# Optimization experiments

Measured on AMD Instinct MI355X. Metric: run time of the kernel, lower is better.

## Reference

```python
import jax, jax.numpy as jnp
import numpy as np

BS, SEQ, D, HEADS = 4, 512, 512, 8

def setup_inputs() -> dict:
    key = jax.random.key(0)
    ks = jax.random.split(key, 11)
    s = 0.02
    return {
        "q": jax.random.normal(ks[0], (BS, SEQ, D), jnp.float32),
        "k": jax.random.normal(ks[1], (BS, SEQ, D), jnp.float32),
        "v": jax.random.normal(ks[2], (BS, SEQ, D), jnp.float32),
        "wq_w": jax.random.normal(ks[3], (D * HEADS, D), jnp.float32) * s,
        "wq_b": jax.random.normal(ks[4], (D * HEADS,), jnp.float32) * s,
        "wk_w": jax.random.normal(ks[5], (D * HEADS, D), jnp.float32) * s,
        "wk_b": jax.random.normal(ks[6], (D * HEADS,), jnp.float32) * s,
        "wv_w": jax.random.normal(ks[7], (D * HEADS, D), jnp.float32) * s,
        "wv_b": jax.random.normal(ks[8], (D * HEADS,), jnp.float32) * s,
        "out_w": jax.random.normal(ks[9], (D, D * HEADS), jnp.float32) * s,
        "out_b": jax.random.normal(ks[10], (D,), jnp.float32) * s,
    }

def reference(q, k, v, wq_w, wq_b, wk_w, wk_b, wv_w, wv_b, out_w, out_b):
    bs, _, d = q.shape
    heads = wq_w.shape[0] // d
    # NOTE: original code applies self.wk to q and self.wq to k (swapped) -- kept faithful.
    # Projections map (bs, seq, d) -> (bs, seq*heads, d): heads folded into sequence axis.
    qp = (q @ wk_w.T + wk_b).reshape(bs, -1, d)  # (bs, L, d), L = seq*heads
    kp = (k @ wq_w.T + wq_b).reshape(bs, -1, d)
    vp = (v @ wv_w.T + wv_b).reshape(bs, -1, d)
    scale = jnp.float32(np.sqrt(d))
    scores = jnp.einsum('bld,bmd->blm', qp, kp) / scale  # (bs, L, L)
    attn = jax.nn.softmax(scores, axis=-1)
    o = jnp.einsum('blm,bmd->bld', attn, vp)             # (bs, L, d)
    o = o.reshape(bs, -1, d * heads)                      # (bs, seq, d*heads)
    return o @ out_w.T + out_b                            # (bs, seq, d)
```

## Files before the change

kernel.cpp:

```cpp
#include <hip/hip_runtime.h>
#include <cstddef>

typedef unsigned short u16;
typedef unsigned char u8;
typedef unsigned u32;
typedef float f32x4 __attribute__((ext_vector_type(4)));
typedef u16 u16x4 __attribute__((ext_vector_type(4)));
typedef u16 u16x8 __attribute__((ext_vector_type(8)));
typedef u8 u8x8 __attribute__((ext_vector_type(8)));
typedef __bf16 bf16x8 __attribute__((ext_vector_type(8)));
typedef int i32x4 __attribute__((ext_vector_type(4)));
typedef int i32x8 __attribute__((ext_vector_type(8)));
typedef long lx2 __attribute__((ext_vector_type(2)));

__device__ __forceinline__ u16 f2bf(float f) {
  u32 u = __builtin_bit_cast(u32, f);
  u += 0x7fffu + ((u >> 16) & 1u);
  return (u16)(u >> 16);
}
__device__ __forceinline__ float bf2f(u16 h) {
  return __builtin_bit_cast(float, ((u32)h) << 16);
}
__device__ __forceinline__ u8 f2fp8(float v) {
  int t = __builtin_amdgcn_cvt_pk_fp8_f32(v, v, 0, false);
  return (u8)(t & 0xff);
}
__device__ __forceinline__ void gld_lds16(const void* g, void* l) {
  __builtin_amdgcn_global_load_lds((const __attribute__((address_space(1))) void*)g,
                                   (__attribute__((address_space(3))) void*)l, 16, 0, 0);
}

__global__ __launch_bounds__(256) void cvt_all(
    const float* __restrict__ q, const float* __restrict__ k, const float* __restrict__ v,
    const float* __restrict__ w5, const float* __restrict__ w3,
    const float* __restrict__ w7, const float* __restrict__ w9,
    u16* __restrict__ o_q, u16* __restrict__ o_k, u16* __restrict__ o_v,
    u16* __restrict__ o_wq, u16* __restrict__ o_wk, u16* __restrict__ o_wv,
    u16* __restrict__ o_ow)
{
  int b = blockIdx.x;
  const float* in; u16* out; int base; bool perm = false;
  if      (b < 512)  { in = q;  out = o_q;  base = b; }
  else if (b < 1024) { in = k;  out = o_k;  base = b - 512; }
  else if (b < 1536) { in = v;  out = o_v;  base = b - 1024; }
  else if (b < 2560) { in = w5; out = o_wq; base = b - 1536; }
  else if (b < 3584) { in = w3; out = o_wk; base = b - 2560; }
  else if (b < 4608) { in = w7; out = o_wv; base = b - 3584; }
  else               { in = w9; out = o_ow; base = b - 4608; perm = true; }
  int i = (base * 256 + threadIdx.x) * 8;
  u16x8 o;
  if (!perm) {
    f32x4 a = *(const f32x4*)(in + i);
    f32x4 c = *(const f32x4*)(in + i + 4);
    o[0] = f2bf(a[0]); o[1] = f2bf(a[1]); o[2] = f2bf(a[2]); o[3] = f2bf(a[3]);
    o[4] = f2bf(c[0]); o[5] = f2bf(c[1]); o[6] = f2bf(c[2]); o[7] = f2bf(c[3]);
  } else {
    int row = i >> 12, col0 = i & 4095;
    int group = col0 & ~63, t0 = col0 & 63;
    const float* rp = in + ((size_t)row << 12) + group;
#pragma unroll
    for (int j = 0; j < 8; ++j) {
      int t = t0 + j;
      o[j] = f2bf(rp[((t & 3) << 4) + (t >> 2)]);
    }
  }
  *(u16x8*)(out + i) = o;
}

__global__ __launch_bounds__(256, 2) void gemm_proj(
    const u16* __restrict__ Aq, const u16* __restrict__ Ak, const u16* __restrict__ Av,
    const u16* __restrict__ Bq, const u16* __restrict__ Bk, const u16* __restrict__ Bv,
    u8* __restrict__ Cq, u8* __restrict__ Ck, u8* __restrict__ Cvv,
    const float* __restrict__ bq, const float* __restrict__ bk, const float* __restrict__ bv,
    int N, int K)
{
  __shared__ alignas(16) char smem[33024];

  const int tid = threadIdx.x, lid = tid & 63, wid = tid >> 6;
  const int wm = wid >> 1, wn = wid & 1;
  const int g = lid >> 4, r16 = lid & 15;
  const int which = blockIdx.z;

  const u16* A = (which == 0) ? Aq : (which == 1) ? Ak : Av;
  const u16* B = (which == 0) ? Bq : (which == 1) ? Bk : Bv;
  u8* C = (which == 0) ? Cq : (which == 1) ? Ck : Cvv;
  const float* bias = (which == 0) ? bq : (which == 1) ? bk : bv;

  const int nx = gridDim.x, ny = gridDim.y;
  const int lin = blockIdx.x + nx * blockIdx.y;
  const int xcd = lin & 7, slot = lin >> 3;
  const int wx = slot % nx;
  const int c_ = xcd + (slot / nx) * 8;
  const int m0 = (c_ % ny) * 128, n0 = wx * 128;

  const int NT = K >> 5;

  int offA[4], offB[4];
#pragma unroll
  for (int f = 0; f < 4; ++f) {
    int ra = wm * 64 + f * 16 + r16;
    offA[f] = ra * 64 + ((g ^ ((ra >> 1) & 3)) << 4);
    int rb = wn * 64 + f * 16 + r16;
    offB[f] = rb * 64 + ((g ^ ((rb >> 1) & 3)) << 4);
  }

  auto stage_tile = [&](int ts) {
    char* base = smem + (ts & 1) * 16384;
    const u16* At = A + (size_t)ts * 32;
    const u16* Bt = B + (size_t)ts * 32;
#pragma unroll
    for (int l = 0; l < 2; ++l) {
      int i = l * 256 + tid;
      int row = i >> 2, x = i & 3;
      int c = x ^ ((row >> 1) & 3);
      gld_lds16(At + (size_t)(m0 + row) * K + c * 8, base + i * 16);
    }
#pragma unroll
    for (int l = 0; l < 2; ++l) {
      int i = l * 256 + tid;
      int row = i >> 2, x = i & 3;
      int c = x ^ ((row >> 1) & 3);
      gld_lds16(Bt + (size_t)(n0 + row) * K + c * 8, base + 8192 + i * 16);
    }
  };

  f32x4 acc[4][4];
#pragma unroll
  for (int i = 0; i < 4; ++i)
#pragma unroll
    for (int j = 0; j < 4; ++j) acc[i][j] = 0.0f;

  stage_tile(0);
  stage_tile(1);
  asm volatile("s_waitcnt vmcnt(4)" ::: "memory");
  __builtin_amdgcn_s_barrier();

  for (int t = 0; t < NT; ++t) {
    const char* Ab = smem + (t & 1) * 16384;
    const char* Bb = Ab + 8192;
    bf16x8 ar[4], br[4];
#pragma unroll
    for (int f = 0; f < 4; ++f) ar[f] = *(const bf16x8*)(Ab + offA[f]);
#pragma unroll
    for (int f = 0; f < 4; ++f) br[f] = *(const bf16x8*)(Bb + offB[f]);
    asm volatile("s_waitcnt lgkmcnt(0)" ::: "memory");
    __builtin_amdgcn_s_barrier();
    if (t + 2 < NT) stage_tile(t + 2);
    __builtin_amdgcn_s_setprio(1);
#pragma unroll
    for (int mf = 0; mf < 4; ++mf)
#pragma unroll
      for (int nf = 0; nf < 4; ++nf)
        acc[mf][nf] = __builtin_amdgcn_mfma_f32_16x16x32_bf16(ar[mf], br[nf], acc[mf][nf], 0, 0, 0);
    __builtin_amdgcn_s_setprio(0);
    if (t + 2 < NT) asm volatile("s_waitcnt vmcnt(4)" ::: "memory");
    else            asm volatile("s_waitcnt vmcnt(0)" ::: "memory");
    __builtin_amdgcn_s_barrier();
  }

  if (which < 2) {
    const int hh = (n0 + wn * 64) >> 9;
    const int d2g = (n0 & 511) + wn * 64;
#pragma unroll
    for (int mf = 0; mf < 4; ++mf)
#pragma unroll
      for (int r = 0; r < 4; ++r) {
        int gm = m0 + wm * 64 + mf * 16 + (g << 2) + r;
        int b = gm >> 9, s = gm & 511;
        float v0 = acc[mf][0][r] + bias[n0 + wn * 64 + 0 * 16 + r16];
        float v1 = acc[mf][1][r] + bias[n0 + wn * 64 + 1 * 16 + r16];
        float v2 = acc[mf][2][r] + bias[n0 + wn * 64 + 2 * 16 + r16];
        float v3 = acc[mf][3][r] + bias[n0 + wn * 64 + 3 * 16 + r16];
        int pk = __builtin_amdgcn_cvt_pk_fp8_f32(v0, v1, 0, false);
        pk = __builtin_amdgcn_cvt_pk_fp8_f32(v2, v3, pk, true);
        int row = (which == 0) ? ((s << 3) + hh) : ((hh << 9) + s);
        *(u32*)(C + (size_t)b * 2097152 + (size_t)row * 512 + d2g + r16 * 4) = (u32)pk;
      }
  } else {
    u16* E = (u16*)smem;
#pragma unroll
    for (int mf = 0; mf < 4; ++mf)
#pragma unroll
      for (int nf = 0; nf < 4; ++nf)
#pragma unroll
        for (int r = 0; r < 4; ++r) {
          int lm = wm * 64 + mf * 16 + (g << 2) + r;
          int ln = wn * 64 + nf * 16 + r16;
          E[lm * 129 + ln] = f2bf(acc[mf][nf][r] + bias[n0 + ln]);
        }
    __syncthreads();
    int b = m0 >> 9, s0 = m0 & 511, hh = n0 >> 9, d20 = n0 & 511;
    int c = tid >> 1;
    int r0 = (tid & 1) * 64;
    u8* dst = C + (size_t)b * 2097152 + (size_t)(d20 + c) * 4096 + (hh << 9) + s0 + r0;
#pragma unroll
    for (int i = 0; i < 64; i += 8) {
      u8x8 p;
#pragma unroll
      for (int jj = 0; jj < 8; ++jj) {
        int t = i + jj;
        int sl = r0 + ((t & 3) << 4) + (t >> 2);
        p[jj] = f2fp8(bf2f(E[sl * 129 + c]));
      }
      *(u8x8*)(dst + i) = p;
    }
  }
}

__global__ __launch_bounds__(256, 4) void gemm_f8s(
    const u8* __restrict__ A, const u8* __restrict__ B, u8* __restrict__ Cv,
    float* __restrict__ Lbuf, int N, int K, float scale,
    long bsA, long bsB, long bsC)
{
  constexpr int SLOT = 256 * 64;
  __shared__ alignas(16) char smem[2 * SLOT];

  const int tid = threadIdx.x, lid = tid & 63, wid = tid >> 6;
  const int wm = wid >> 1, wn = wid & 1;
  const int g = lid >> 4, r16 = lid & 15;

  const int nx = gridDim.x, ny = gridDim.y;
  const int lin = blockIdx.x + nx * (blockIdx.y + ny * blockIdx.z);
  const int xcd = lin & 7, slot = lin >> 3;
  const int wx = slot % nx;
  const int c_ = xcd + (slot / nx) * 8;
  const int m0 = (c_ % ny) * 128, n0 = wx * 128, z = c_ / ny;

  A += (size_t)z * bsA;
  B += (size_t)z * bsB;
  const int NT = K >> 6;

  int offA[4], offB[4];
#pragma unroll
  for (int f = 0; f < 4; ++f) {
    int ra = wm * 64 + f * 16 + r16;
    offA[f] = ra * 64 + ((g ^ ((ra >> 1) & 3)) << 4);
    int rb = wn * 64 + f * 16 + r16;
    offB[f] = rb * 64 + ((g ^ ((rb >> 1) & 3)) << 4);
  }

  auto stage_tile = [&](int ts) {
    char* base = smem + (ts & 1) * SLOT;
    const u8* At = A + (size_t)ts * 64;
    const u8* Bt = B + (size_t)ts * 64;
#pragma unroll
    for (int l = 0; l < 2; ++l) {
      int i = l * 256 + tid;
      int row = i >> 2, x = i & 3;
      int c = x ^ ((row >> 1) & 3);
      gld_lds16(At + (size_t)(m0 + row) * K + c * 16, base + i * 16);
    }
#pragma unroll
    for (int l = 0; l < 2; ++l) {
      int i = l * 256 + tid;
      int row = i >> 2, x = i & 3;
      int c = x ^ ((row >> 1) & 3);
      gld_lds16(Bt + (size_t)(n0 + row) * K + c * 16, base + 8192 + i * 16);
    }
  };

  f32x4 acc[4][4];
#pragma unroll
  for (int i = 0; i < 4; ++i)
#pragma unroll
    for (int j = 0; j < 4; ++j) acc[i][j] = 0.0f;

  stage_tile(0);
  stage_tile(1);
  asm volatile("s_waitcnt vmcnt(4)" ::: "memory");
  __builtin_amdgcn_s_barrier();

  for (int t = 0; t < NT; ++t) {
    const char* Ab = smem + (t & 1) * SLOT;
    const char* Bb = Ab + 8192;
    lx2 ar[4], br[4];
#pragma unroll
    for (int f = 0; f < 4; ++f) ar[f] = *(const lx2*)(Ab + offA[f]);
#pragma unroll
    for (int f = 0; f < 4; ++f) br[f] = *(const lx2*)(Bb + offB[f]);
    asm volatile("s_waitcnt lgkmcnt(0)" ::: "memory");
    __builtin_amdgcn_s_barrier();
    if (t + 2 < NT) stage_tile(t + 2);
    __builtin_amdgcn_s_setprio(1);
#pragma unroll
    for (int mf = 0; mf < 4; ++mf)
#pragma unroll
      for (int nf = 0; nf < 4; ++nf) {
        acc[mf][nf] = __builtin_amdgcn_mfma_f32_16x16x32_fp8_fp8(ar[mf][0], br[nf][0], acc[mf][nf], 0, 0, 0);
        acc[mf][nf] = __builtin_amdgcn_mfma_f32_16x16x32_fp8_fp8(ar[mf][1], br[nf][1], acc[mf][nf], 0, 0, 0);
      }
    __builtin_amdgcn_s_setprio(0);
    if (t + 2 < NT) asm volatile("s_waitcnt vmcnt(4)" ::: "memory");
    else            asm volatile("s_waitcnt vmcnt(0)" ::: "memory");
    __builtin_amdgcn_s_barrier();
  }

  u8* Cp = Cv + (size_t)z * bsC;
  float* Lp = Lbuf + (size_t)z * 4096;
#pragma unroll
  for (int mf = 0; mf < 4; ++mf) {
#pragma unroll
    for (int r = 0; r < 4; ++r) {
      int gm = m0 + wm * 64 + mf * 16 + (g << 2) + r;
      float p0 = __expf(acc[mf][0][r] * scale);
      float p1 = __expf(acc[mf][1][r] * scale);
      float p2 = __expf(acc[mf][2][r] * scale);
      float p3 = __expf(acc[mf][3][r] * scale);
      float rs = (p0 + p1) + (p2 + p3);
      int pk = __builtin_amdgcn_cvt_pk_fp8_f32(p0, p1, 0, false);
      pk = __builtin_amdgcn_cvt_pk_fp8_f32(p2, p3, pk, true);
      *(u32*)(Cp + (size_t)gm * N + n0 + wn * 64 + r16 * 4) = (u32)pk;
      rs += __shfl_xor(rs, 1); rs += __shfl_xor(rs, 2);
      rs += __shfl_xor(rs, 4); rs += __shfl_xor(rs, 8);
      if (r16 == 0) atomicAdd(&Lp[gm], rs);
    }
  }
}

__global__ __launch_bounds__(512, 4) void gemm_mx_pv(
    const u8* __restrict__ A, const u8* __restrict__ B, u16* __restrict__ Cv,
    const float* __restrict__ Lbuf, int N, int K,
    long bsA, long bsB, long bsC)
{
  __shared__ alignas(16) char smem[65536];

  const int tid = threadIdx.x, lid = tid & 63, wid = tid >> 6;
  const int wm = wid >> 1, wn = wid & 1;
  const int g = lid >> 4, r16 = lid & 15;

  const int nx = gridDim.x, ny = gridDim.y;
  const int lin = blockIdx.x + nx * (blockIdx.y + ny * blockIdx.z);
  const int xcd = lin & 7, slot = lin >> 3;
  const int wx = slot % nx;
  const int c_ = xcd + (slot / nx) * 8;
  const int m0 = (c_ % ny) * 128, n0 = wx * 128, z = c_ / ny;

  A += (size_t)z * bsA;
  B += (size_t)z * bsB;
  const int NT = K >> 7;

  int offA[2], offB[4];
#pragma unroll
  for (int f = 0; f < 2; ++f) {
    int ra = wm * 32 + f * 16 + r16;
    offA[f] = ra * 64 + ((g ^ ((ra >> 1) & 3)) << 4);
  }
#pragma unroll
  for (int f = 0; f < 4; ++f) {
    int rb = wn * 64 + f * 16 + r16;
    offB[f] = rb * 64 + ((g ^ ((rb >> 1) & 3)) << 4);
  }

  auto stage_tile = [&](int ts) {
    char* base = smem + (ts & 1) * 32768;
    const u8* At = A + (size_t)ts * 128;
    const u8* Bt = B + (size_t)ts * 128;
#pragma unroll
    for (int l = 0; l < 2; ++l) {
      int i = l * 512 + tid;
      int half = i >> 9, rem = i & 511, row = rem >> 2, x = rem & 3;
      int c = x ^ ((row >> 1) & 3);
      gld_lds16(At + (size_t)(m0 + row) * K + half * 64 + c * 16,
                base + half * 8192 + rem * 16);
    }
#pragma unroll
    for (int l = 0; l < 2; ++l) {
      int i = l * 512 + tid;
      int half = i >> 9, rem = i & 511, row = rem >> 2, x = rem & 3;
      int c = x ^ ((row >> 1) & 3);
      gld_lds16(Bt + (size_t)(n0 + row) * K + half * 64 + c * 16,
                base + 16384 + half * 8192 + rem * 16);
    }
  };

  f32x4 acc[2][4];
#pragma unroll
  for (int i = 0; i < 2; ++i)
#pragma unroll
    for (int j = 0; j < 4; ++j) acc[i][j] = 0.0f;

  stage_tile(0);
  stage_tile(1);
  asm volatile("s_waitcnt vmcnt(4)" ::: "memory");
  __builtin_amdgcn_s_barrier();

  for (int t = 0; t < NT; ++t) {
    const char* Ab = smem + (t & 1) * 32768;
    const char* Bb = Ab + 16384;
    i32x8 af[2], bfr[4];
#pragma unroll
    for (int f = 0; f < 2; ++f) {
      i32x4 lo = *(const i32x4*)(Ab + offA[f]);
      i32x4 hi = *(const i32x4*)(Ab + 8192 + offA[f]);
      af[f] = __builtin_shufflevector(lo, hi, 0, 1, 2, 3, 4, 5, 6, 7);
    }
#pragma unroll
    for (int f = 0; f < 4; ++f) {
      i32x4 lo = *(const i32x4*)(Bb + offB[f]);
      i32x4 hi = *(const i32x4*)(Bb + 8192 + offB[f]);
      bfr[f] = __builtin_shufflevector(lo, hi, 0, 1, 2, 3, 4, 5, 6, 7);
    }
    asm volatile("s_waitcnt lgkmcnt(0)" ::: "memory");
    __builtin_amdgcn_s_barrier();
    if (t + 2 < NT) stage_tile(t + 2);
    __builtin_amdgcn_s_setprio(1);
#pragma unroll
    for (int mf = 0; mf < 2; ++mf)
#pragma unroll
      for (int nf = 0; nf < 4; ++nf)
        acc[mf][nf] = __builtin_amdgcn_mfma_scale_f32_16x16x128_f8f6f4(
            af[mf], bfr[nf], acc[mf][nf],
            0 , 0 ,
            0, 0x7F7F7F7F , 0, 0x7F7F7F7F );
    __builtin_amdgcn_s_setprio(0);
    if (t + 2 < NT) asm volatile("s_waitcnt vmcnt(4)" ::: "memory");
    else            asm volatile("s_waitcnt vmcnt(0)" ::: "memory");
    __builtin_amdgcn_s_barrier();
  }

  u16* C = Cv + (size_t)z * bsC;
  const float* Lp = Lbuf + (size_t)z * 4096;
#pragma unroll
  for (int mf = 0; mf < 2; ++mf) {
#pragma unroll
    for (int r = 0; r < 4; ++r) {
      int gm = m0 + wm * 32 + mf * 16 + (g << 2) + r;
      float inv = 1.0f / Lp[gm];
      u16x4 o;
#pragma unroll
      for (int nf = 0; nf < 4; ++nf) o[nf] = f2bf(acc[mf][nf][r] * inv);
      *(u16x4*)(C + (size_t)(gm >> 3) * 4096 + (size_t)(gm & 7) * 512 +
                n0 + wn * 64 + r16 * 4) = o;
    }
  }
}

__global__ __launch_bounds__(256) void gemm_bt_final(
    const u16* __restrict__ A, const u16* __restrict__ B, float* __restrict__ C,
    const float* __restrict__ bias, int N, int K)
{
  constexpr int BM = 64, BN = 64, BK = 64;
  __shared__ alignas(16) char smem[(BM + BN) * BK * 2];
  u16* As = (u16*)smem;
  u16* Bs = As + BM * BK;

  const int tid = threadIdx.x;
  const int lid = tid & 63, wid = tid >> 6;
  const int m0 = blockIdx.y * BM, n0 = blockIdx.x * BN;
  const int wm = wid >> 1, wn = wid & 1;

  f32x4 acc[2][2];
#pragma unroll
  for (int i = 0; i < 2; ++i)
#pragma unroll
    for (int j = 0; j < 2; ++j) acc[i][j] = 0.0f;

  const int rA = lid >> 3;
  const int ke = (lid & 7) * 8;

  const int nK = K / BK;
  for (int kt = 0; kt < nK; ++kt) {
    const int k0 = kt * BK;
#pragma unroll
    for (int c = 0; c < 2; ++c) {
      int chunk = wid * 2 + c;
      gld_lds16(A + (size_t)(m0 + chunk * 8 + rA) * K + k0 + ke, (char*)As + chunk * 1024);
    }
#pragma unroll
    for (int c = 0; c < 2; ++c) {
      int chunk = wid * 2 + c;
      gld_lds16(B + (size_t)(n0 + chunk * 8 + rA) * K + k0 + ke, (char*)Bs + chunk * 1024);
    }
    __syncthreads();
#pragma unroll
    for (int kc = 0; kc < 2; ++kc) {
      bf16x8 af[2], bfv[2];
      const int kb = kc * 32 + (lid >> 4) * 8;
#pragma unroll
      for (int i = 0; i < 2; ++i)
        af[i] = *(const bf16x8*)&As[(wm * 32 + i * 16 + (lid & 15)) * BK + kb];
#pragma unroll
      for (int j = 0; j < 2; ++j)
        bfv[j] = *(const bf16x8*)&Bs[(wn * 32 + j * 16 + (lid & 15)) * BK + kb];
#pragma unroll
      for (int i = 0; i < 2; ++i)
#pragma unroll
        for (int j = 0; j < 2; ++j)
          acc[i][j] = __builtin_amdgcn_mfma_f32_16x16x32_bf16(af[i], bfv[j], acc[i][j], 0, 0, 0);
    }
    __syncthreads();
  }

#pragma unroll
  for (int i = 0; i < 2; ++i)
#pragma unroll
    for (int j = 0; j < 2; ++j)
#pragma unroll
      for (int r = 0; r < 4; ++r) {
        int gm = m0 + wm * 32 + i * 16 + ((lid >> 4) << 2) + r;
        int gn = n0 + wn * 32 + j * 16 + (lid & 15);
        C[(size_t)gm * N + gn] = acc[i][j][r] + bias[gn];
      }
}

extern "C" void kernel_launch(void* const* d_in, const int* in_sizes, int n_in,
                              void* d_out, int out_size, void* d_ws, size_t ws_size,
                              hipStream_t stream) {
  (void)in_sizes; (void)n_in; (void)out_size; (void)ws_size;
  const float* q_f  = (const float*)d_in[0];
  const float* k_f  = (const float*)d_in[1];
  const float* v_f  = (const float*)d_in[2];
  const float* wq_b = (const float*)d_in[4];
  const float* wk_b = (const float*)d_in[6];
  const float* wv_b = (const float*)d_in[8];
  const float* ou_b = (const float*)d_in[10];
  float* out = (float*)d_out;

  char* ws = (char*)d_ws;
  u16* q_bf  = (u16*)(ws + 0);
  u16* k_bf  = (u16*)(ws + 2097152);
  u16* v_bf  = (u16*)(ws + 4194304);
  u16* wA_q  = (u16*)(ws + 6291456);
  u16* wA_k  = (u16*)(ws + 10485760);
  u16* wA_v  = (u16*)(ws + 14680064);
  u16* ow_bf = (u16*)(ws + 18874368);
  u8*  qp    = (u8*)(ws + 23068672);
  u8*  kp    = (u8*)(ws + 31457280);
  u8*  vpt   = (u8*)(ws + 39845888);
  u16* oflat = (u16*)(ws + 48234496);
  u8*  P     = (u8*)(ws + 65011712);

  float* L = (float*)d_out;

  cvt_all<<<5632, 256, 0, stream>>>(
      q_f, k_f, v_f, (const float*)d_in[5], (const float*)d_in[3],
      (const float*)d_in[7], (const float*)d_in[9],
      q_bf, k_bf, v_bf, wA_q, wA_k, wA_v, ow_bf);

  gemm_proj<<<dim3(32,16,3), 256, 0, stream>>>(
      q_bf, k_bf, v_bf, wA_q, wA_k, wA_v, qp, kp, vpt, wk_b, wq_b, wv_b, 4096, 512);

  const float scl = 0.04419417382415922f;
  hipMemsetAsync(L, 0, 65536, stream);
  gemm_f8s<<<dim3(32,32,4), 256, 0, stream>>>(qp, kp, P, L, 4096, 512, scl,
                                              2097152, 2097152, 16777216);
  gemm_mx_pv<<<dim3(4,32,4), 512, 0, stream>>>(P, vpt, oflat, L, 512, 4096,
                                               16777216, 2097152, 2097152);
  gemm_bt_final<<<dim3(8,32,1), 256, 0, stream>>>(oflat, ow_bf, out, ou_b, 512, 4096);
}
```

Measured before the change: 206.2 us.

## Split-K final projection with larger tiles, and fold L zeroing into convert kernel

The final output projection (M=2048, N=512, K=4096) moves from a 64x64-tile kernel that loops over the full K to a split-K kernel. It uses 128x128 tiles, double-buffered swizzled LDS staging and four K partitions written as fp32 partials, and a separate reduce kernel adds the partials and the bias. The memset of the L buffer is removed and one extra block of the convert kernel zeroes it instead, saving an API call. The gain is more MFMA work per block and better pipelining, at the cost of extra partial-sum traffic and one more launch.

```diff
diff --git a/kernel.cpp b/kernel.cpp
--- a/kernel.cpp
+++ b/kernel.cpp
@@ -36,9 +36,16 @@
     const float* __restrict__ w7, const float* __restrict__ w9,
     u16* __restrict__ o_q, u16* __restrict__ o_k, u16* __restrict__ o_v,
     u16* __restrict__ o_wq, u16* __restrict__ o_wk, u16* __restrict__ o_wv,
-    u16* __restrict__ o_ow)
+    u16* __restrict__ o_ow, float* __restrict__ Lz)
 {
   int b = blockIdx.x;
+  if (b >= 5632) {
+    f32x4 z4 = 0.0f;
+    float* p = Lz + threadIdx.x * 64;
+#pragma unroll
+    for (int j = 0; j < 16; ++j) *(f32x4*)(p + j * 4) = z4;
+    return;
+  }
   const float* in; u16* out; int base; bool perm = false;
   if      (b < 512)  { in = q;  out = o_q;  base = b; }
   else if (b < 1024) { in = k;  out = o_k;  base = b - 512; }
@@ -410,8 +417,7 @@
       for (int nf = 0; nf < 4; ++nf)
         acc[mf][nf] = __builtin_amdgcn_mfma_scale_f32_16x16x128_f8f6f4(
             af[mf], bfr[nf], acc[mf][nf],
-            0 , 0 ,
-            0, 0x7F7F7F7F , 0, 0x7F7F7F7F );
+            0, 0, 0, 0x7F7F7F7F, 0, 0x7F7F7F7F);
     __builtin_amdgcn_s_setprio(0);
     if (t + 2 < NT) asm volatile("s_waitcnt vmcnt(4)" ::: "memory");
     else            asm volatile("s_waitcnt vmcnt(0)" ::: "memory");
@@ -435,72 +441,108 @@
   }
 }
 
-__global__ __launch_bounds__(256) void gemm_bt_final(
-    const u16* __restrict__ A, const u16* __restrict__ B, float* __restrict__ C,
-    const float* __restrict__ bias, int N, int K)
+__global__ __launch_bounds__(256, 2) void gemm_fpart(
+    const u16* __restrict__ A0, const u16* __restrict__ B0,
+    float* __restrict__ part, int K)
 {
-  constexpr int BM = 64, BN = 64, BK = 64;
-  __shared__ alignas(16) char smem[(BM + BN) * BK * 2];
-  u16* As = (u16*)smem;
-  u16* Bs = As + BM * BK;
-
-  const int tid = threadIdx.x;
-  const int lid = tid & 63, wid = tid >> 6;
-  const int m0 = blockIdx.y * BM, n0 = blockIdx.x * BN;
+  __shared__ alignas(16) char smem[32768];
+
+  const int tid = threadIdx.x, lid = tid & 63, wid = tid >> 6;
   const int wm = wid >> 1, wn = wid & 1;
-
-  f32x4 acc[2][2];
-#pragma unroll
-  for (int i = 0; i < 2; ++i)
-#pragma unroll
-    for (int j = 0; j < 2; ++j) acc[i][j] = 0.0f;
-
-  const int rA = lid >> 3;
-  const int ke = (lid & 7) * 8;
-
-  const int nK = K / BK;
-  for (int kt = 0; kt < nK; ++kt) {
-    const int k0 = kt * BK;
-#pragma unroll
-    for (int c = 0; c < 2; ++c) {
-      int chunk = wid * 2 + c;
-      gld_lds16(A + (size_t)(m0 + chunk * 8 + rA) * K + k0 + ke, (char*)As + chunk * 1024);
-    }
-#pragma unroll
-    for (int c = 0; c < 2; ++c) {
-      int chunk = wid * 2 + c;
-      gld_lds16(B + (size_t)(n0 + chunk * 8 + rA) * K + k0 + ke, (char*)Bs + chunk * 1024);
-    }
-    __syncthreads();
-#pragma unroll
-    for (int kc = 0; kc < 2; ++kc) {
-      bf16x8 af[2], bfv[2];
-      const int kb = kc * 32 + (lid >> 4) * 8;
-#pragma unroll
-      for (int i = 0; i < 2; ++i)
-        af[i] = *(const bf16x8*)&As[(wm * 32 + i * 16 + (lid & 15)) * BK + kb];
-#pragma unroll
-      for (int j = 0; j < 2; ++j)
-        bfv[j] = *(const bf16x8*)&Bs[(wn * 32 + j * 16 + (lid & 15)) * BK + kb];
-#pragma unroll
-      for (int i = 0; i < 2; ++i)
-#pragma unroll
-        for (int j = 0; j < 2; ++j)
-          acc[i][j] = __builtin_amdgcn_mfma_f32_16x16x32_bf16(af[i], bfv[j], acc[i][j], 0, 0, 0);
-    }
-    __syncthreads();
-  }
-
-#pragma unroll
-  for (int i = 0; i < 2; ++i)
-#pragma unroll
-    for (int j = 0; j < 2; ++j)
+  const int g = lid >> 4, r16 = lid & 15;
+  const int m0 = blockIdx.y * 128, n0 = blockIdx.x * 128, z = blockIdx.z;
+
+  const u16* A = A0 + (size_t)z * 1024;
+  const u16* B = B0 + (size_t)z * 1024;
+  constexpr int NT = 32;
+
+  int offA[4], offB[4];
+#pragma unroll
+  for (int f = 0; f < 4; ++f) {
+    int ra = wm * 64 + f * 16 + r16;
+    offA[f] = ra * 64 + ((g ^ ((ra >> 1) & 3)) << 4);
+    int rb = wn * 64 + f * 16 + r16;
+    offB[f] = rb * 64 + ((g ^ ((rb >> 1) & 3)) << 4);
+  }
+
+  auto stage_tile = [&](int ts) {
+    char* base = smem + (ts & 1) * 16384;
+    const u16* At = A + (size_t)ts * 32;
+    const u16* Bt = B + (size_t)ts * 32;
+#pragma unroll
+    for (int l = 0; l < 2; ++l) {
+      int i = l * 256 + tid;
+      int row = i >> 2, x = i & 3;
+      int c = x ^ ((row >> 1) & 3);
+      gld_lds16(At + (size_t)(m0 + row) * K + c * 8, base + i * 16);
+    }
+#pragma unroll
+    for (int l = 0; l < 2; ++l) {
+      int i = l * 256 + tid;
+      int row = i >> 2, x = i & 3;
+      int c = x ^ ((row >> 1) & 3);
+      gld_lds16(Bt + (size_t)(n0 + row) * K + c * 8, base + 8192 + i * 16);
+    }
+  };
+
+  f32x4 acc[4][4];
+#pragma unroll
+  for (int i = 0; i < 4; ++i)
+#pragma unroll
+    for (int j = 0; j < 4; ++j) acc[i][j] = 0.0f;
+
+  stage_tile(0);
+  stage_tile(1);
+  asm volatile("s_waitcnt vmcnt(4)" ::: "memory");
+  __builtin_amdgcn_s_barrier();
+
+  for (int t = 0; t < NT; ++t) {
+    const char* Ab = smem + (t & 1) * 16384;
+    const char* Bb = Ab + 8192;
+    bf16x8 ar[4], br[4];
+#pragma unroll
+    for (int f = 0; f < 4; ++f) ar[f] = *(const bf16x8*)(Ab + offA[f]);
+#pragma unroll
+    for (int f = 0; f < 4; ++f) br[f] = *(const bf16x8*)(Bb + offB[f]);
+    asm volatile("s_waitcnt lgkmcnt(0)" ::: "memory");
+    __builtin_amdgcn_s_barrier();
+    if (t + 2 < NT) stage_tile(t + 2);
+    __builtin_amdgcn_s_setprio(1);
+#pragma unroll
+    for (int mf = 0; mf < 4; ++mf)
+#pragma unroll
+      for (int nf = 0; nf < 4; ++nf)
+        acc[mf][nf] = __builtin_amdgcn_mfma_f32_16x16x32_bf16(ar[mf], br[nf], acc[mf][nf], 0, 0, 0);
+    __builtin_amdgcn_s_setprio(0);
+    if (t + 2 < NT) asm volatile("s_waitcnt vmcnt(4)" ::: "memory");
+    else            asm volatile("s_waitcnt vmcnt(0)" ::: "memory");
+    __builtin_amdgcn_s_barrier();
+  }
+
+  float* P = part + ((size_t)z << 20);
+#pragma unroll
+  for (int mf = 0; mf < 4; ++mf)
+#pragma unroll
+    for (int nf = 0; nf < 4; ++nf)
 #pragma unroll
       for (int r = 0; r < 4; ++r) {
-        int gm = m0 + wm * 32 + i * 16 + ((lid >> 4) << 2) + r;
-        int gn = n0 + wn * 32 + j * 16 + (lid & 15);
-        C[(size_t)gm * N + gn] = acc[i][j][r] + bias[gn];
+        int gm = m0 + wm * 64 + mf * 16 + (g << 2) + r;
+        int gn = n0 + wn * 64 + nf * 16 + r16;
+        P[(size_t)gm * 512 + gn] = acc[mf][nf][r];
       }
+}
+
+__global__ __launch_bounds__(256) void fin_reduce(
+    const float* __restrict__ part, const float* __restrict__ bias,
+    float* __restrict__ out)
+{
+  int i = (blockIdx.x * 256 + threadIdx.x) * 4;
+  f32x4 s = *(const f32x4*)(part + i);
+  s += *(const f32x4*)(part + 1048576 + i);
+  s += *(const f32x4*)(part + 2097152 + i);
+  s += *(const f32x4*)(part + 3145728 + i);
+  s += *(const f32x4*)(bias + (i & 511));
+  *(f32x4*)(out + i) = s;
 }
 
 extern "C" void kernel_launch(void* const* d_in, const int* in_sizes, int n_in,
@@ -529,22 +571,23 @@
   u8*  vpt   = (u8*)(ws + 39845888);
   u16* oflat = (u16*)(ws + 48234496);
   u8*  P     = (u8*)(ws + 65011712);
+  float* fpt = (float*)(ws + 132120576);
 
   float* L = (float*)d_out;
 
-  cvt_all<<<5632, 256, 0, stream>>>(
+  cvt_all<<<5633, 256, 0, stream>>>(
       q_f, k_f, v_f, (const float*)d_in[5], (const float*)d_in[3],
       (const float*)d_in[7], (const float*)d_in[9],
-      q_bf, k_bf, v_bf, wA_q, wA_k, wA_v, ow_bf);
+      q_bf, k_bf, v_bf, wA_q, wA_k, wA_v, ow_bf, L);
 
   gemm_proj<<<dim3(32,16,3), 256, 0, stream>>>(
       q_bf, k_bf, v_bf, wA_q, wA_k, wA_v, qp, kp, vpt, wk_b, wq_b, wv_b, 4096, 512);
 
   const float scl = 0.04419417382415922f;
-  hipMemsetAsync(L, 0, 65536, stream);
   gemm_f8s<<<dim3(32,32,4), 256, 0, stream>>>(qp, kp, P, L, 4096, 512, scl,
                                               2097152, 2097152, 16777216);
   gemm_mx_pv<<<dim3(4,32,4), 512, 0, stream>>>(P, vpt, oflat, L, 512, 4096,
                                                16777216, 2097152, 2097152);
-  gemm_bt_final<<<dim3(8,32,1), 256, 0, stream>>>(oflat, ow_bf, out, ou_b, 512, 4096);
-}
+  gemm_fpart<<<dim3(4,16,4), 256, 0, stream>>>(oflat, ow_bf, fpt, 4096);
+  fin_reduce<<<1024, 256, 0, stream>>>(fpt, ou_b, out);
+}
```

New measurement: 178.6 us (median of 2 runs). 1.15x faster.
